# Performance work log

Measured on AMD Instinct MI355X. Metric: run time of the kernel, lower is better.

The kernel has to match this reference:

```python
import jax, jax.numpy as jnp
import numpy as np

N_NODES = 100000
N_EDGES = 1200000
NFEAT, NHID, NCLASS = 64, 256, 40
DROP_RATE = 0.5
ORDER = 8


def setup_inputs() -> dict:
    key = jax.random.key(0)
    k = jax.random.split(key, 6)
    x = jax.random.normal(k[0], (N_NODES, NFEAT), dtype=jnp.float32)
    edge_index = jax.random.randint(k[1], (2, N_EDGES), 0, N_NODES, dtype=jnp.int64)
    stdv1 = 1.0 / np.sqrt(NHID)
    stdv2 = 1.0 / np.sqrt(NCLASS)
    W1 = jax.random.normal(k[2], (NFEAT, NHID), dtype=jnp.float32) * stdv1
    b1 = jax.random.normal(k[3], (NHID,), dtype=jnp.float32) * stdv1
    W2 = jax.random.normal(k[4], (NHID, NCLASS), dtype=jnp.float32) * stdv2
    b2 = jax.random.normal(k[5], (NCLASS,), dtype=jnp.float32) * stdv2
    return {"x": x, "edge_index": edge_index, "W1": W1, "b1": b1, "W2": W2, "b2": b2}


def _norm_adj(edge_index, n):
    # A + I, then D^{-1/2} (A+I) D^{-1/2}  (GCN symmetric normalization)
    loops = jnp.arange(n, dtype=edge_index.dtype)
    row = jnp.concatenate([edge_index[0], loops])
    col = jnp.concatenate([edge_index[1], loops])
    ones = jnp.ones(row.shape[0], dtype=jnp.float32)
    deg = jax.ops.segment_sum(ones, row, num_segments=n)  # row sums (self-loops guarantee deg>=1)
    d_inv_sqrt = 1.0 / jnp.sqrt(deg)
    ew = d_inv_sqrt[row] * d_inv_sqrt[col]  # [E+N] edge weights
    return row, col, ew


def reference(x, edge_index, W1, b1, W2, b2):
    n = x.shape[0]
    row, col, ew = _norm_adj(edge_index, n)

    def spmm(h):  # out[row] += ew * h[col]
        return jax.ops.segment_sum(ew[:, None] * h[col], row, num_segments=n)

    # eval-mode input scaling (training=False branch of GRAND.forward)
    h = x * (1.0 - DROP_RATE)
    y = h
    for _ in range(ORDER):
        h = spmm(h)
        y = y + h
    y = y / (ORDER + 1.0)

    # MLP in eval mode: dropouts are no-ops, use_bn=False
    hid = jax.nn.relu(y @ W1 + b1)
    return hid @ W2 + b2
```

## Files before the change

kernel.cpp:

```cpp
#include <hip/hip_runtime.h>

#define NN 100000
#define NE 1200000
#define NF 64
#define NH 256
#define NC 40
#define ORDER_C 8
#define BINB 1024
#define BCAP 165000
#define NSB 782
#define SBROWS 128
#define SBCAP 1920
#define CCAP (NE + 7 * NN)

typedef __attribute__((ext_vector_type(8))) short short8;
typedef __attribute__((ext_vector_type(4))) float f32x4;

__device__ __forceinline__ unsigned bf16r(float x) {
    unsigned u = __float_as_uint(x);
    return (u + 0x7FFFu + ((u >> 16) & 1u)) >> 16;
}
__device__ __forceinline__ unsigned packbf(float lo, float hi) {
    return bf16r(lo) | (bf16r(hi) << 16);
}
__device__ __forceinline__ float bflo(unsigned u) { return __uint_as_float(u << 16); }
__device__ __forceinline__ float bfhi(unsigned u) { return __uint_as_float(u & 0xFFFF0000u); }


static __global__ __launch_bounds__(256) void k_bin(const int* __restrict__ rows,
                                                    const int* __restrict__ cols,
                                                    int* __restrict__ bcnt,
                                                    int* __restrict__ browb,
                                                    int* __restrict__ bcolb, int E)
{
    __shared__ int rbuf[BINB];
    __shared__ unsigned short lofs[BINB];
    __shared__ int hist[8], basew[8];
    int t = threadIdx.x;
    int e0 = blockIdx.x * BINB;
    int m = E - e0; if (m > BINB) m = BINB;
    if (t < 8) hist[t] = 0;
    __syncthreads();
    for (int i = t; i < m; i += 256) {
        int r = rows[e0 + i];
        rbuf[i] = r;
        int b = r / 12500;
        lofs[i] = (unsigned short)atomicAdd(&hist[b], 1);
    }
    __syncthreads();
    if (t < 8) basew[t] = atomicAdd(&bcnt[t], hist[t]);
    __syncthreads();
    for (int i = t; i < m; i += 256) {
        int r = rbuf[i];
        int b = r / 12500;
        size_t pos = (size_t)b * BCAP + basew[b] + lofs[i];
        browb[pos] = r;
        bcolb[pos] = cols[e0 + i];
    }
}


static __global__ __launch_bounds__(256) void k_bin98(const int* __restrict__ browb,
                                                      const int* __restrict__ bcolb,
                                                      const int* __restrict__ bcnt,
                                                      int* __restrict__ sbcnt,
                                                      int* __restrict__ sbrow,
                                                      int* __restrict__ sbcol)
{
    __shared__ int rbuf[2048];
    __shared__ unsigned short lofs[2048];
    __shared__ int hist[NSB], basew[NSB];
    int t = threadIdx.x;
    int b = blockIdx.x & 7;
    int m = bcnt[b];
    const int* srcr = browb + (size_t)b * BCAP;
    const int* srcc = bcolb + (size_t)b * BCAP;
    int stride = (gridDim.x >> 3) * 2048;
    for (int base = (blockIdx.x >> 3) * 2048; base < m; base += stride) {
        int cm = m - base; if (cm > 2048) cm = 2048;
        for (int s = t; s < NSB; s += 256) hist[s] = 0;
        __syncthreads();
        for (int i = t; i < cm; i += 256) {
            int r = srcr[base + i];
            rbuf[i] = r;
            lofs[i] = (unsigned short)atomicAdd(&hist[r >> 7], 1);
        }
        __syncthreads();
        for (int s = t; s < NSB; s += 256) {
            int h = hist[s];
            basew[s] = h ? atomicAdd(&sbcnt[s], h) : 0;
        }
        __syncthreads();
        for (int i = t; i < cm; i += 256) {
            int r = rbuf[i];
            int sb = r >> 7;
            int pos = sb * SBCAP + basew[sb] + lofs[i];
            sbrow[pos] = r;
            sbcol[pos] = srcc[base + i];
        }
        __syncthreads();
    }
}


static __global__ __launch_bounds__(256) void k_hist(const int* __restrict__ sbrow,
                                                     const int* __restrict__ sbcnt,
                                                     int* __restrict__ ghist,
                                                     int* __restrict__ sbtot)
{
    __shared__ int h[SBROWS];
    __shared__ int red[256];
    int sb = blockIdx.x;
    int t = threadIdx.x;
    int m = sbcnt[sb];
    const int* src = sbrow + (size_t)sb * SBCAP;
    if (t < SBROWS) h[t] = 0;
    __syncthreads();
    for (int i = t; i < m; i += 256) atomicAdd(&h[src[i] & 127], 1);
    __syncthreads();
    int pad = 0;
    if (t < SBROWS) {
        ghist[sb * SBROWS + t] = h[t];
        pad = (h[t] + 7) & ~7;
    }
    red[t] = pad;
    __syncthreads();
    for (int off = 128; off > 0; off >>= 1) {
        if (t < off) red[t] += red[t + off];
        __syncthreads();
    }
    if (t == 0) sbtot[sb] = red[0];
}


static __global__ __launch_bounds__(1024) void k_scansb(const int* __restrict__ sbtot,
                                                        int* __restrict__ sbbase,
                                                        int* __restrict__ rp, int n)
{
    __shared__ int red[1024];
    int t = threadIdx.x;
    int v = (t < NSB) ? sbtot[t] : 0;
    red[t] = v;
    __syncthreads();
    for (int off = 1; off < 1024; off <<= 1) {
        int x = (t >= off) ? red[t - off] : 0;
        __syncthreads();
        red[t] += x;
        __syncthreads();
    }
    if (t < NSB) sbbase[t] = (t == 0) ? 0 : red[t - 1];
    if (t == NSB - 1) rp[n] = red[t];
}


static __global__ __launch_bounds__(256) void k_csr(const int* __restrict__ sbrow,
                                                    const int* __restrict__ sbcol,
                                                    const int* __restrict__ sbcnt,
                                                    const int* __restrict__ ghist,
                                                    const int* __restrict__ sbbase,
                                                    int* __restrict__ rp,
                                                    float2* __restrict__ drd,
                                                    int* __restrict__ ccol, int n)
{
    __shared__ int rb[SBCAP];
    __shared__ int cb[SBCAP];
    __shared__ int sc[SBROWS], ro[SBROWS], fl[SBROWS];
    int sb = blockIdx.x;
    int t = threadIdx.x;
    int m = sbcnt[sb];
    const int* srcr = sbrow + (size_t)sb * SBCAP;
    const int* srcc = sbcol + (size_t)sb * SBCAP;
    for (int i = t; i < m; i += 256) { rb[i] = srcr[i] & 127; cb[i] = srcc[i]; }
    int h = (t < SBROWS) ? ghist[sb * SBROWS + t] : 0;
    if (t < SBROWS) { sc[t] = (h + 7) & ~7; fl[t] = 0; }
    __syncthreads();
    for (int off = 1; off < SBROWS; off <<= 1) {
        int x = (t >= off && t < SBROWS) ? sc[t - off] : 0;
        __syncthreads();
        if (t < SBROWS) sc[t] += x;
        __syncthreads();
    }
    int base = sbbase[sb];
    if (t < SBROWS) {
        ro[t] = (t == 0) ? 0 : sc[t - 1];
        int row = sb * SBROWS + t;
        if (row < n) {
            rp[row] = base + ro[t];
            float d1 = rsqrtf((float)(h + 1));
            drd[row] = make_float2(d1, (float)(h + 1) * d1);
            int p = (h + 7) & ~7;
            for (int q = h; q < p; ++q) ccol[base + ro[t] + q] = n;
        }
    }
    __syncthreads();
    for (int i = t; i < m; i += 256) {
        int r = rb[i];
        int rank = atomicAdd(&fl[r], 1);
        ccol[base + ro[r] + rank] = cb[i];
    }
}


static __global__ __launch_bounds__(256) void k_pack(const float* __restrict__ W1,
                                                     const float* __restrict__ W2,
                                                     unsigned short* __restrict__ w1f,
                                                     unsigned short* __restrict__ w2f)
{
    int t = blockIdx.x * 256 + threadIdx.x;
    if (t < 2048) {
        int lane = t & 63;
        int g = lane >> 4, col = (lane & 15) + ((t >> 6) & 15) * 16;
        int s = t >> 10;
        unsigned short* p = w1f + (size_t)t * 8;
        #pragma unroll
        for (int e = 0; e < 8; ++e) {
            int k = 32 * s + 8 * g + e;
            p[e] = (unsigned short)bf16r(W1[k * NH + col]);
        }
    } else if (t < 2048 + 1536) {
        int u = t - 2048;
        int lane = u & 63;
        int tile = u >> 6;
        int nt = tile % 3, s = tile / 3;
        int g = lane >> 4, col = (lane & 15) + nt * 16;
        unsigned short* p = w2f + (size_t)u * 8;
        #pragma unroll
        for (int e = 0; e < 8; ++e) {
            int k = 32 * s + 8 * g + e;
            p[e] = (col < NC) ? (unsigned short)bf16r(W2[k * NC + col]) : 0;
        }
    }
}


static __global__ __launch_bounds__(256) void k_init(const float4* __restrict__ x4,
                                                     float4* __restrict__ y4,
                                                     uint4* __restrict__ ga,
                                                     uint4* __restrict__ gbp,
                                                     const float2* __restrict__ drd,
                                                     int nchunk)
{
    int i = blockIdx.x * 256 + threadIdx.x;
    if (i >= nchunk) {
        if (i < nchunk + 8) {
            uint4 z = make_uint4(0, 0, 0, 0);
            ga[i] = z; gbp[i] = z;
        }
        return;
    }
    float d1 = drd[i >> 3].x;
    float4 a = x4[i * 2], b = x4[i * 2 + 1];
    a.x *= 0.5f; a.y *= 0.5f; a.z *= 0.5f; a.w *= 0.5f;
    b.x *= 0.5f; b.y *= 0.5f; b.z *= 0.5f; b.w *= 0.5f;
    y4[i * 2] = a; y4[i * 2 + 1] = b;
    ga[i] = make_uint4(packbf(a.x * d1, a.y * d1), packbf(a.z * d1, a.w * d1),
                       packbf(b.x * d1, b.y * d1), packbf(b.z * d1, b.w * d1));
}


template<bool ACC, bool WRITEG>
static __global__ __launch_bounds__(256) void k_spmm(const uint2* __restrict__ gb,
                                                     uint2* __restrict__ go,
                                                     float4* __restrict__ y4,
                                                     const int* __restrict__ rp,
                                                     const int* __restrict__ ccol,
                                                     const float2* __restrict__ drd, int n)
{
    int wid  = (blockIdx.x * 256 + threadIdx.x) >> 6;
    int lane = threadIdx.x & 63;
    int row  = wid * 4 + (lane >> 4);
    int j    = lane & 15;
    if (row >= n) return;
    int s = rp[row], e = rp[row + 1];

    float a0 = 0.f, a1 = 0.f, a2 = 0.f, a3 = 0.f;
    float b0 = 0.f, b1 = 0.f, b2 = 0.f, b3 = 0.f;
    for (int i = s; i < e; i += 8) {
        int4 cA = *(const int4*)&ccol[i];
        int4 cB = *(const int4*)&ccol[i + 4];
        uint2 h0 = gb[(size_t)cA.x * 16 + j];
        uint2 h1 = gb[(size_t)cA.y * 16 + j];
        uint2 h2 = gb[(size_t)cA.z * 16 + j];
        uint2 h3 = gb[(size_t)cA.w * 16 + j];
        uint2 h4 = gb[(size_t)cB.x * 16 + j];
        uint2 h5 = gb[(size_t)cB.y * 16 + j];
        uint2 h6 = gb[(size_t)cB.z * 16 + j];
        uint2 h7 = gb[(size_t)cB.w * 16 + j];
        a0 += bflo(h0.x); a1 += bfhi(h0.x); a2 += bflo(h0.y); a3 += bfhi(h0.y);
        b0 += bflo(h1.x); b1 += bfhi(h1.x); b2 += bflo(h1.y); b3 += bfhi(h1.y);
        a0 += bflo(h2.x); a1 += bfhi(h2.x); a2 += bflo(h2.y); a3 += bfhi(h2.y);
        b0 += bflo(h3.x); b1 += bfhi(h3.x); b2 += bflo(h3.y); b3 += bfhi(h3.y);
        a0 += bflo(h4.x); a1 += bfhi(h4.x); a2 += bflo(h4.y); a3 += bfhi(h4.y);
        b0 += bflo(h5.x); b1 += bfhi(h5.x); b2 += bflo(h5.y); b3 += bfhi(h5.y);
        a0 += bflo(h6.x); a1 += bfhi(h6.x); a2 += bflo(h6.y); a3 += bfhi(h6.y);
        b0 += bflo(h7.x); b1 += bfhi(h7.x); b2 += bflo(h7.y); b3 += bfhi(h7.y);
    }

    float2 dr = drd[row];
    uint2 gs = gb[(size_t)row * 16 + j];
    float g0 = bflo(gs.x), g1 = bfhi(gs.x), g2 = bflo(gs.y), g3 = bfhi(gs.y);
    float s0 = (a0 + b0) + g0;
    float s1 = (a1 + b1) + g1;
    float s2 = (a2 + b2) + g2;
    float s3 = (a3 + b3) + g3;
    float h0 = dr.x * s0, h1 = dr.x * s1, h2 = dr.x * s2, h3 = dr.x * s3;
    if (WRITEG)
        go[(size_t)row * 16 + j] = make_uint2(packbf(dr.x * h0, dr.x * h1),
                                              packbf(dr.x * h2, dr.x * h3));
    if (ACC) {
        float4 yv = y4[(size_t)row * 16 + j];
        yv.x += fmaf(g0, dr.y, h0);
        yv.y += fmaf(g1, dr.y, h1);
        yv.z += fmaf(g2, dr.y, h2);
        yv.w += fmaf(g3, dr.y, h3);
        y4[(size_t)row * 16 + j] = yv;
    }
}


#define YSTR 72
#define HSTR 264

static __global__ __launch_bounds__(256) void k_mlp(const float4* __restrict__ y4,
                                                    const short8* __restrict__ w1f,
                                                    const short8* __restrict__ w2f,
                                                    const float* __restrict__ b1,
                                                    const float* __restrict__ b2,
                                                    float* __restrict__ out, int n)
{
    __shared__ short lds[64 * HSTR];
    int t = threadIdx.x;
    int lane = t & 63;
    int w = t >> 6;
    int base = blockIdx.x * 64;
    const float S = 1.f / 9.f;

    {
        int r = t >> 2, q = t & 3;
        int row = base + r;
        unsigned v[8];
        if (row < n) {
            const float4* yp = y4 + (size_t)row * 16 + q * 4;
            #pragma unroll
            for (int i = 0; i < 4; ++i) {
                float4 f = yp[i];
                v[i * 2]     = packbf(f.x * S, f.y * S);
                v[i * 2 + 1] = packbf(f.z * S, f.w * S);
            }
        } else {
            #pragma unroll
            for (int i = 0; i < 8; ++i) v[i] = 0;
        }
        uint4* dst = (uint4*)&lds[r * YSTR + q * 16];
        dst[0] = make_uint4(v[0], v[1], v[2], v[3]);
        dst[1] = make_uint4(v[4], v[5], v[6], v[7]);
    }
    __syncthreads();

    int m = lane & 15, g = lane >> 4;

    f32x4 acc[4][4];
    {
        short8 a[4][2];
        #pragma unroll
        for (int mt = 0; mt < 4; ++mt)
            #pragma unroll
            for (int s = 0; s < 2; ++s)
                a[mt][s] = *(const short8*)&lds[(mt * 16 + m) * YSTR + s * 32 + g * 8];
        #pragma unroll
        for (int nt4 = 0; nt4 < 4; ++nt4) {
            int nt = w * 4 + nt4;
            short8 b0  = w1f[nt * 64 + lane];
            short8 b1v = w1f[(16 + nt) * 64 + lane];
            float bias = b1[nt * 16 + m];
            #pragma unroll
            for (int mt = 0; mt < 4; ++mt) {
                f32x4 c = {bias, bias, bias, bias};
                c = __builtin_amdgcn_mfma_f32_16x16x32_bf16(a[mt][0], b0,  c, 0, 0, 0);
                c = __builtin_amdgcn_mfma_f32_16x16x32_bf16(a[mt][1], b1v, c, 0, 0, 0);
                acc[mt][nt4] = c;
            }
        }
    }
    __syncthreads();

    {
        #pragma unroll
        for (int mt = 0; mt < 4; ++mt)
            #pragma unroll
            for (int nt4 = 0; nt4 < 4; ++nt4) {
                int col = w * 64 + nt4 * 16 + m;
                #pragma unroll
                for (int r = 0; r < 4; ++r) {
                    float hv = fmaxf(acc[mt][nt4][r], 0.f);
                    lds[(mt * 16 + g * 4 + r) * HSTR + col] = (short)bf16r(hv);
                }
            }
    }
    __syncthreads();

    {
        short8 a2[8];
        #pragma unroll
        for (int s = 0; s < 8; ++s)
            a2[s] = *(const short8*)&lds[(w * 16 + m) * HSTR + s * 32 + g * 8];
        #pragma unroll
        for (int nt = 0; nt < 3; ++nt) {
            int col = nt * 16 + m;
            float bias = (col < NC) ? b2[col] : 0.f;
            f32x4 c = {bias, bias, bias, bias};
            #pragma unroll
            for (int s = 0; s < 8; ++s)
                c = __builtin_amdgcn_mfma_f32_16x16x32_bf16(a2[s], w2f[(s * 3 + nt) * 64 + lane], c, 0, 0, 0);
            if (col < NC) {
                #pragma unroll
                for (int r = 0; r < 4; ++r) {
                    int row = base + w * 16 + g * 4 + r;
                    if (row < n) out[(size_t)row * NC + col] = c[r];
                }
            }
        }
    }
}


extern "C" void kernel_launch(void* const* d_in, const int* in_sizes, int n_in,
                              void* d_out, int out_size, void* d_ws, size_t ws_size,
                              hipStream_t stream)
{
    const float* x  = (const float*)d_in[0];
    const int*   ei = (const int*)d_in[1];
    const float* W1 = (const float*)d_in[2];
    const float* b1 = (const float*)d_in[3];
    const float* W2 = (const float*)d_in[4];
    const float* b2 = (const float*)d_in[5];
    float* out = (float*)d_out;

    const int n = NN, E = NE;

    char* ws = (char*)d_ws;
    size_t off = 0;
    auto alloc = [&](size_t bytes) -> void* {
        void* p = ws + off;
        off = (off + bytes + 255) & ~(size_t)255;
        return p;
    };
    int*    rp     = (int*)   alloc((size_t)(n + 1) * 4);
    float2* drd    = (float2*)alloc((size_t)n * 8);
    int*    bcnt   = (int*)   alloc(8 * 4);
    int*    sbcnt  = (int*)   alloc(NSB * 4);
    int*    sbtot  = (int*)   alloc(NSB * 4);
    int*    sbbase = (int*)   alloc(NSB * 4);
    int*    browb  = (int*)   alloc((size_t)8 * BCAP * 4);
    int*    bcolb  = (int*)   alloc((size_t)8 * BCAP * 4);
    int*    sbrow  = (int*)   alloc((size_t)NSB * SBCAP * 4);
    int*    sbcol  = (int*)   alloc((size_t)NSB * SBCAP * 4);
    int*    ghist  = (int*)   alloc((size_t)NSB * SBROWS * 4);
    int*    ccol   = (int*)   alloc((size_t)CCAP * 4);
    unsigned short* w1f = (unsigned short*)alloc(2048 * 8 * 2);
    unsigned short* w2f = (unsigned short*)alloc(1536 * 8 * 2);
    uint4* ha   = (uint4*)alloc((size_t)(n + 1) * NF * 2);
    uint4* hbuf = (uint4*)alloc((size_t)(n + 1) * NF * 2);
    float* y    = (float*)alloc((size_t)n * NF * 4);

    hipMemsetAsync(bcnt, 0, 8 * 4, stream);
    hipMemsetAsync(sbcnt, 0, NSB * 4, stream);

    const int* rows = ei;
    const int* cols = ei + E;

    k_bin   <<<(E + BINB - 1) / BINB, 256, 0, stream>>>(rows, cols, bcnt, browb, bcolb, E);
    k_bin98 <<<640, 256, 0, stream>>>(browb, bcolb, bcnt, sbcnt, sbrow, sbcol);
    k_hist  <<<NSB, 256, 0, stream>>>(sbrow, sbcnt, ghist, sbtot);
    k_scansb<<<1, 1024, 0, stream>>>(sbtot, sbbase, rp, n);
    k_csr   <<<NSB, 256, 0, stream>>>(sbrow, sbcol, sbcnt, ghist, sbbase, rp, drd, ccol, n);
    k_pack  <<<14, 256, 0, stream>>>(W1, W2, w1f, w2f);

    int nchunk = n * 8;
    k_init<<<(nchunk + 8 + 255) / 256, 256, 0, stream>>>((const float4*)x, (float4*)y,
                                                         ha, hbuf, drd, nchunk);

    uint4* cur = ha;
    uint4* nxt = hbuf;
    int spmm_blocks = (n + 15) / 16;
    for (int it = 0; it < ORDER_C; ++it) {
        bool acc = (it & 1) != 0;
        bool wg  = (it != ORDER_C - 1);
        if (acc && wg)
            k_spmm<true, true><<<spmm_blocks, 256, 0, stream>>>((const uint2*)cur, (uint2*)nxt,
                                                                (float4*)y, rp, ccol, drd, n);
        else if (acc)
            k_spmm<true, false><<<spmm_blocks, 256, 0, stream>>>((const uint2*)cur, (uint2*)nxt,
                                                                 (float4*)y, rp, ccol, drd, n);
        else
            k_spmm<false, true><<<spmm_blocks, 256, 0, stream>>>((const uint2*)cur, (uint2*)nxt,
                                                                 (float4*)y, rp, ccol, drd, n);
        uint4* tswap = cur; cur = nxt; nxt = tswap;
    }

    k_mlp<<<(n + 63) / 64, 256, 0, stream>>>((const float4*)y, (const short8*)w1f,
                                             (const short8*)w2f, b1, b2, out, n);
}
```

Before: 328.6 us.

## Fuse all propagation steps into one cooperative persistent kernel with grid syncs

Replaces the eight separate SpMM launches with a single cooperative kernel. Each thread owns up to seven feature slots across all eight steps and keeps its running y accumulator and its own row's current value in registers, with a grid-wide sync between steps. This removes the per-launch gaps and the repeated global read-modify-write of y, and drops the self-row reload. In exchange it pays seven grid barriers, runs at the lower occupancy set by launch bounds, and seeds y from the bf16-rounded scaled input rather than the fp32 copy. It falls back to the old per-step launches when the occupancy query says the grid won't fit.

Result: no change. 328.8 us (+0.1%).

```diff
diff --git a/kernel.cpp b/kernel.cpp
--- a/kernel.cpp
+++ b/kernel.cpp
@@ -1,4 +1,7 @@
 #include <hip/hip_runtime.h>
+#include <hip/hip_cooperative_groups.h>
+
+namespace cg = cooperative_groups;
 
 #define NN 100000
 #define NE 1200000
@@ -12,6 +15,7 @@
 #define SBROWS 128
 #define SBCAP 1920
 #define CCAP (NE + 7 * NN)
+#define MAXS 7
 
 typedef __attribute__((ext_vector_type(8))) short short8;
 typedef __attribute__((ext_vector_type(4))) float f32x4;
@@ -258,24 +262,14 @@
 }
 
 
-template<bool ACC, bool WRITEG>
-static __global__ __launch_bounds__(256) void k_spmm(const uint2* __restrict__ gb,
-                                                     uint2* __restrict__ go,
-                                                     float4* __restrict__ y4,
-                                                     const int* __restrict__ rp,
-                                                     const int* __restrict__ ccol,
-                                                     const float2* __restrict__ drd, int n)
-{
-    int wid  = (blockIdx.x * 256 + threadIdx.x) >> 6;
-    int lane = threadIdx.x & 63;
-    int row  = wid * 4 + (lane >> 4);
-    int j    = lane & 15;
-    if (row >= n) return;
-    int s = rp[row], e = rp[row + 1];
-
+__device__ __forceinline__ void gather_row(const uint2* __restrict__ gb,
+                                           const int* __restrict__ ccol,
+                                           int e0, int e1, int j,
+                                           float& o0, float& o1, float& o2, float& o3)
+{
     float a0 = 0.f, a1 = 0.f, a2 = 0.f, a3 = 0.f;
     float b0 = 0.f, b1 = 0.f, b2 = 0.f, b3 = 0.f;
-    for (int i = s; i < e; i += 8) {
+    for (int i = e0; i < e1; i += 8) {
         int4 cA = *(const int4*)&ccol[i];
         int4 cB = *(const int4*)&ccol[i + 4];
         uint2 h0 = gb[(size_t)cA.x * 16 + j];
@@ -295,14 +289,99 @@
         a0 += bflo(h6.x); a1 += bfhi(h6.x); a2 += bflo(h6.y); a3 += bfhi(h6.y);
         b0 += bflo(h7.x); b1 += bfhi(h7.x); b2 += bflo(h7.y); b3 += bfhi(h7.y);
     }
-
+    o0 = a0 + b0; o1 = a1 + b1; o2 = a2 + b2; o3 = a3 + b3;
+}
+
+
+static __global__ __launch_bounds__(256, 4)
+void k_prop(uint2* __restrict__ gA, uint2* __restrict__ gB,
+            float4* __restrict__ y4,
+            const int* __restrict__ rp, const int* __restrict__ ccol,
+            const float2* __restrict__ drd, int n)
+{
+    cg::grid_group grid = cg::this_grid();
+    const int T = gridDim.x * 256;
+    const int tid = blockIdx.x * 256 + threadIdx.x;
+    const int nslots = n * 16;
+
+    float4 yacc[MAXS];
+    uint2  own[MAXS];
+
+    #pragma unroll
+    for (int s = 0; s < MAXS; ++s) {
+        int slot = tid + s * T;
+        yacc[s] = make_float4(0.f, 0.f, 0.f, 0.f);
+        own[s] = make_uint2(0u, 0u);
+        if (slot < nslots) {
+            int row = slot >> 4;
+            uint2 gv = gA[slot];
+            own[s] = gv;
+            float rd = drd[row].y;
+            yacc[s].x = bflo(gv.x) * rd;
+            yacc[s].y = bfhi(gv.x) * rd;
+            yacc[s].z = bflo(gv.y) * rd;
+            yacc[s].w = bfhi(gv.y) * rd;
+        }
+    }
+
+    uint2* cur = gA;
+    uint2* nxt = gB;
+
+    for (int r = 0; r < ORDER_C; ++r) {
+        #pragma unroll
+        for (int s = 0; s < MAXS; ++s) {
+            int slot = tid + s * T;
+            if (slot < nslots) {
+                int row = slot >> 4;
+                int j = slot & 15;
+                float s0, s1, s2, s3;
+                gather_row(cur, ccol, rp[row], rp[row + 1], j, s0, s1, s2, s3);
+                float2 dr = drd[row];
+                s0 += bflo(own[s].x); s1 += bfhi(own[s].x);
+                s2 += bflo(own[s].y); s3 += bfhi(own[s].y);
+                float h0 = dr.x * s0, h1 = dr.x * s1;
+                float h2 = dr.x * s2, h3 = dr.x * s3;
+                yacc[s].x += h0; yacc[s].y += h1;
+                yacc[s].z += h2; yacc[s].w += h3;
+                uint2 gnew = make_uint2(packbf(dr.x * h0, dr.x * h1),
+                                        packbf(dr.x * h2, dr.x * h3));
+                own[s] = gnew;
+                if (r != ORDER_C - 1) nxt[slot] = gnew;
+            }
+        }
+        if (r != ORDER_C - 1) {
+            grid.sync();
+            uint2* t2 = cur; cur = nxt; nxt = t2;
+        }
+    }
+
+    #pragma unroll
+    for (int s = 0; s < MAXS; ++s) {
+        int slot = tid + s * T;
+        if (slot < nslots) y4[slot] = yacc[s];
+    }
+}
+
+
+template<bool ACC, bool WRITEG>
+static __global__ __launch_bounds__(256) void k_spmm(const uint2* __restrict__ gb,
+                                                     uint2* __restrict__ go,
+                                                     float4* __restrict__ y4,
+                                                     const int* __restrict__ rp,
+                                                     const int* __restrict__ ccol,
+                                                     const float2* __restrict__ drd, int n)
+{
+    int wid  = (blockIdx.x * 256 + threadIdx.x) >> 6;
+    int lane = threadIdx.x & 63;
+    int row  = wid * 4 + (lane >> 4);
+    int j    = lane & 15;
+    if (row >= n) return;
+    float s0, s1, s2, s3;
+    gather_row(gb, ccol, rp[row], rp[row + 1], j, s0, s1, s2, s3);
     float2 dr = drd[row];
     uint2 gs = gb[(size_t)row * 16 + j];
     float g0 = bflo(gs.x), g1 = bfhi(gs.x), g2 = bflo(gs.y), g3 = bfhi(gs.y);
-    float s0 = (a0 + b0) + g0;
-    float s1 = (a1 + b1) + g1;
-    float s2 = (a2 + b2) + g2;
-    float s3 = (a3 + b3) + g3;
+    s0 += g0; s1 += g1; s2 += g2; s3 += g3;
     float h0 = dr.x * s0, h1 = dr.x * s1, h2 = dr.x * s2, h3 = dr.x * s3;
     if (WRITEG)
         go[(size_t)row * 16 + j] = make_uint2(packbf(dr.x * h0, dr.x * h1),
@@ -480,22 +559,44 @@
     k_init<<<(nchunk + 8 + 255) / 256, 256, 0, stream>>>((const float4*)x, (float4*)y,
                                                          ha, hbuf, drd, nchunk);
 
-    uint4* cur = ha;
-    uint4* nxt = hbuf;
-    int spmm_blocks = (n + 15) / 16;
-    for (int it = 0; it < ORDER_C; ++it) {
-        bool acc = (it & 1) != 0;
-        bool wg  = (it != ORDER_C - 1);
-        if (acc && wg)
-            k_spmm<true, true><<<spmm_blocks, 256, 0, stream>>>((const uint2*)cur, (uint2*)nxt,
-                                                                (float4*)y, rp, ccol, drd, n);
-        else if (acc)
-            k_spmm<true, false><<<spmm_blocks, 256, 0, stream>>>((const uint2*)cur, (uint2*)nxt,
-                                                                 (float4*)y, rp, ccol, drd, n);
-        else
-            k_spmm<false, true><<<spmm_blocks, 256, 0, stream>>>((const uint2*)cur, (uint2*)nxt,
-                                                                 (float4*)y, rp, ccol, drd, n);
-        uint4* tswap = cur; cur = nxt; nxt = tswap;
+    int nslots = n * 16;
+    int nbPerCU = 0;
+    hipOccupancyMaxActiveBlocksPerMultiprocessor(&nbPerCU, k_prop, 256, 0);
+    int capacity = nbPerCU * 256;
+    int needed = (nslots + 256 * MAXS - 1) / (256 * MAXS);
+
+    if (capacity >= needed && capacity > 0) {
+        int grid = capacity;
+        int maxg = (nslots + 255) / 256;
+        if (grid > maxg) grid = maxg;
+        uint2* gAp = (uint2*)ha;
+        uint2* gBp = (uint2*)hbuf;
+        float4* yp = (float4*)y;
+        const int* rpp = rp;
+        const int* ccolp = ccol;
+        const float2* drdp = drd;
+        int nv = n;
+        void* args[] = { (void*)&gAp, (void*)&gBp, (void*)&yp,
+                         (void*)&rpp, (void*)&ccolp, (void*)&drdp, (void*)&nv };
+        hipLaunchCooperativeKernel((void*)k_prop, dim3(grid), dim3(256), args, 0, stream);
+    } else {
+        uint4* cur = ha;
+        uint4* nxt = hbuf;
+        int spmm_blocks = (n + 15) / 16;
+        for (int it = 0; it < ORDER_C; ++it) {
+            bool acc = (it & 1) != 0;
+            bool wg  = (it != ORDER_C - 1);
+            if (acc && wg)
+                k_spmm<true, true><<<spmm_blocks, 256, 0, stream>>>((const uint2*)cur, (uint2*)nxt,
+                                                                    (float4*)y, rp, ccol, drd, n);
+            else if (acc)
+                k_spmm<true, false><<<spmm_blocks, 256, 0, stream>>>((const uint2*)cur, (uint2*)nxt,
+                                                                     (float4*)y, rp, ccol, drd, n);
+            else
+                k_spmm<false, true><<<spmm_blocks, 256, 0, stream>>>((const uint2*)cur, (uint2*)nxt,
+                                                                     (float4*)y, rp, ccol, drd, n);
+            uint4* tswap = cur; cur = nxt; nxt = tswap;
+        }
     }
 
     k_mlp<<<(n + 63) / 64, 256, 0, stream>>>((const float4*)y, (const short8*)w1f,
```
